# Performance work log

Measured on AMD Instinct MI355X. Metric: run time of the kernel, lower is better.

Reference implementation:

```python
import jax, jax.numpy as jnp
import numpy as np

ALPHA = 0.1        # ista() default lambda (module-level alpha is unused in this path)
N_ITERS = 50       # fixed iteration count replacing tolerance-based early exit
POWER_ITERS = 20   # power iterations to estimate Lipschitz constant L = ||Wd||_2^2


def _soft_threshold(x, t):
    return jnp.sign(x) * jnp.maximum(jnp.abs(x) - t, 0.0)


def _lipschitz(Wd):
    # largest eigenvalue of Wd^T Wd via power iteration
    v = jnp.ones((Wd.shape[1],), Wd.dtype)
    def body(v, _):
        v = Wd.T @ (Wd @ v)
        v = v / (jnp.linalg.norm(v) + 1e-12)
        return v, None
    v, _ = jax.lax.scan(body, v, None, length=POWER_ITERS)
    return jnp.vdot(v, Wd.T @ (Wd @ v)) / (jnp.vdot(v, v) + 1e-12)


def _ista(X, Wd):
    # X: [B, D], Wd: [D, K] -> sparse codes Z: [B, K]
    L = jax.lax.stop_gradient(_lipschitz(Wd))
    step = 1.0 / L
    Z0 = jnp.zeros((X.shape[0], Wd.shape[1]), X.dtype)
    def body(Z, _):
        grad = (Z @ Wd.T - X) @ Wd          # [B,D] @ [D,K] -> [B,K]
        Z = _soft_threshold(Z - step * grad, step * ALPHA)
        return Z, None
    Z, _ = jax.lax.scan(body, Z0, None, length=N_ITERS)
    return Z


def setup_inputs() -> dict:
    key = jax.random.key(0)
    k1, k2 = jax.random.split(key)
    z_e_x = jax.random.normal(k1, (8192, 16, 8, 8), jnp.float32)   # [B,C,H,W]
    dictionary = jax.random.normal(k2, (1024, 512), jnp.float32)   # [D,K], D=H*W*C
    return {"z_e_x": z_e_x, "dictionary": dictionary}


def reference(z_e_x, dictionary):
    B = z_e_x.shape[0]
    # permute(0,2,3,1).flatten(start_dim=1): [B,C,H,W] -> [B, H*W*C]
    X = jnp.transpose(z_e_x, (0, 2, 3, 1)).reshape(B, -1)
    Z = _ista(X, dictionary)                                  # [B,K]
    sparsity = jnp.sum(jnp.abs(Z) > 1e-6) / B
    outputs = (dictionary @ Z.T).T                            # [B,D]
    # torch code views back to z_e_x.shape WITHOUT inverse permute; replicate exactly
    return outputs.reshape(z_e_x.shape), sparsity
```

## Files before the change

### kernel.cpp

```cpp
#include <hip/hip_runtime.h>
#include <math.h>

#define BATCH 8192
#define DIM 1024
#define KDIM 512
#define ALPHA_C 0.1f
#define N_ITERS 50
#define ROWS 32
#define ZSH 512
#define SEG 256
#define SH 32.0f
#define SZ 16.0f
#define INVS 0.001953125f

typedef short bf16x8 __attribute__((ext_vector_type(8)));
typedef float f32x4 __attribute__((ext_vector_type(4)));
typedef long longx2 __attribute__((ext_vector_type(2)));

__device__ __forceinline__ short f2bf(float x) {
  union { float f; unsigned u; } v; v.f = x;
  unsigned r = v.u + 0x7fffu + ((v.u >> 16) & 1u);
  return (short)(r >> 16);
}
__device__ __forceinline__ float bf2f(short s) {
  union { float f; unsigned u; } v;
  v.u = ((unsigned)(unsigned short)s) << 16;
  return v.f;
}

__device__ __forceinline__ int zswz(int row, int col) {
  return row * ZSH + ((((col >> 3) ^ (row & 15)) << 3) | (col & 7));
}
__device__ __forceinline__ int zoff8(int row, int colg) {
  return row * ZSH + ((colg ^ (row & 15)) << 3);
}
__device__ __forceinline__ int z8a(int row, int c) {
  int g = ((((c >> 3) & 3) << 4) | (c >> 5)) ^ (row & 14);
  return row * 512 + g * 8 + (c & 7);
}

__global__ __launch_bounds__(256) void k_mmT_part(const float* __restrict__ A,
                                                  const float* __restrict__ B,
                                                  float* __restrict__ P) {
  int tx = (threadIdx.x & 15) * 2;
  int ty = (threadIdx.x >> 4) * 2;
  int a0 = blockIdx.y * 32 + ty;
  int b0 = blockIdx.x * 32 + tx;
  int j0 = blockIdx.z * SEG;
  float a00 = 0.f, a01 = 0.f, a10 = 0.f, a11 = 0.f;
  for (int j = j0; j < j0 + SEG; j += 8) {
#pragma unroll
    for (int u = 0; u < 8; ++u) {
      float2 av = *(const float2*)&A[(size_t)(j + u) * KDIM + a0];
      float2 bv = *(const float2*)&B[(size_t)(j + u) * KDIM + b0];
      a00 += av.x * bv.x;
      a01 += av.x * bv.y;
      a10 += av.y * bv.x;
      a11 += av.y * bv.y;
    }
  }
  float* P0 = P + (size_t)blockIdx.z * KDIM * KDIM;
  *(float2*)&P0[(size_t)a0 * KDIM + b0] = make_float2(a00, a01);
  *(float2*)&P0[(size_t)(a0 + 1) * KDIM + b0] = make_float2(a10, a11);
}

__global__ __launch_bounds__(256) void k_red(const float* __restrict__ P,
                                             float* __restrict__ C, int S,
                                             float scale) {
  int t = blockIdx.x * 256 + threadIdx.x;
  f32x4 s = (f32x4){0.f, 0.f, 0.f, 0.f};
  for (int z = 0; z < S; ++z) {
    f32x4 p = *(const f32x4*)&P[(size_t)z * KDIM * KDIM + t * 4];
    s.x += p.x; s.y += p.y; s.z += p.z; s.w += p.w;
  }
  s.x *= scale; s.y *= scale; s.z *= scale; s.w *= scale;
  *(f32x4*)&C[t * 4] = s;
}

__global__ __launch_bounds__(1024) void k_power_fast(
    const float* __restrict__ G4, const float* __restrict__ G8,
    const float* __restrict__ G, float* __restrict__ scal) {
  __shared__ float v[KDIM];
  __shared__ float part[1024];
  __shared__ double red[16];
  __shared__ double red2[16];
  __shared__ float stot;
  int tid = threadIdx.x;
  int lane = tid & 63, wid = tid >> 6;
  int col = tid & 511, h = tid >> 9;
  if (h == 0) v[col] = 1.0f;
  __syncthreads();

  const float* mats[3] = {G4, G8, G8};
#pragma unroll
  for (int s = 0; s < 3; ++s) {
    const float* gp = mats[s] + (size_t)(h * 256) * KDIM + col;
    const float* vp = v + h * 256;
    float a0 = 0.f, a1 = 0.f, a2 = 0.f, a3 = 0.f;
#pragma unroll 4
    for (int j = 0; j < 256; j += 4) {
      a0 += gp[(size_t)(j + 0) * KDIM] * vp[j + 0];
      a1 += gp[(size_t)(j + 1) * KDIM] * vp[j + 1];
      a2 += gp[(size_t)(j + 2) * KDIM] * vp[j + 2];
      a3 += gp[(size_t)(j + 3) * KDIM] * vp[j + 3];
    }
    part[tid] = (a0 + a1) + (a2 + a3);
    __syncthreads();
    float u = 0.f;
    double ssq = 0.0;
    if (h == 0) {
      u = part[col] + part[col + 512];
      ssq = (double)u * (double)u;
    }
#pragma unroll
    for (int off = 32; off; off >>= 1) ssq += __shfl_xor(ssq, off);
    if (lane == 0) red[wid] = ssq;
    __syncthreads();
    if (tid == 0) {
      double t = 0.0;
      for (int i = 0; i < 16; ++i) t += red[i];
      stot = (float)(sqrt(t) + 1e-12);
    }
    __syncthreads();
    if (h == 0) v[col] = u / stot;
    __syncthreads();
  }

  {
    const float* gp = G + (size_t)(h * 256) * KDIM + col;
    const float* vp = v + h * 256;
    float a0 = 0.f, a1 = 0.f, a2 = 0.f, a3 = 0.f;
#pragma unroll 4
    for (int j = 0; j < 256; j += 4) {
      a0 += gp[(size_t)(j + 0) * KDIM] * vp[j + 0];
      a1 += gp[(size_t)(j + 1) * KDIM] * vp[j + 1];
      a2 += gp[(size_t)(j + 2) * KDIM] * vp[j + 2];
      a3 += gp[(size_t)(j + 3) * KDIM] * vp[j + 3];
    }
    part[tid] = (a0 + a1) + (a2 + a3);
    __syncthreads();
    double nu = 0.0, de = 0.0;
    if (h == 0) {
      float u = part[col] + part[col + 512];
      nu = (double)v[col] * (double)u;
      de = (double)v[col] * (double)v[col];
    }
#pragma unroll
    for (int off = 32; off; off >>= 1) {
      nu += __shfl_xor(nu, off);
      de += __shfl_xor(de, off);
    }
    if (lane == 0) { red[wid] = nu; red2[wid] = de; }
    __syncthreads();
    if (tid == 0) {
      double n = 0.0, d = 0.0;
      for (int i = 0; i < 16; ++i) { n += red[i]; d += red2[i]; }
      float L = (float)(n / (d + 1e-12));
      float step = 1.0f / L;
      scal[0] = step;
      scal[1] = step * ALPHA_C;
    }
  }
}

__global__ __launch_bounds__(256) void k_pack_h8(const float* __restrict__ G,
                                                 const float* __restrict__ scal,
                                                 char* __restrict__ H8,
                                                 float* __restrict__ hd) {
  int t = blockIdx.x * 256 + threadIdx.x;
  int k = t >> 9, n = t & 511;
  float step = scal[0];
  float g = G[k * KDIM + n];
  if (k == n) hd[n] = 1.0f - step * g;
  float h = (k == n) ? 0.f : (-step * g) * SH;
  int p = __builtin_amdgcn_cvt_pk_fp8_f32(h, h, 0, false);
  size_t off = ((size_t)((k >> 5) * 4 + ((k >> 3) & 3))) * 4096 + n * 8 + (k & 7);
  H8[off] = (char)(p & 0xff);
}

__global__ __launch_bounds__(256) void k_pack_w(const float* __restrict__ Wd,
                                                const float* __restrict__ scal,
                                                short* __restrict__ Wh) {
  int t = blockIdx.x * 256 + threadIdx.x;
  int k = t >> 9, n = t & 511;
  float w = scal[0] * Wd[k * KDIM + n];
  int kk = k >> 5, q = (k >> 3) & 3, j = k & 7;
  Wh[((size_t)((kk * 4 + q) * 512 + n)) * 8 + j] = f2bf(w);
}

__global__ __launch_bounds__(256) void k_pack_wt(const float* __restrict__ Wd,
                                                 short* __restrict__ Wh) {
  int t = blockIdx.x * 256 + threadIdx.x;
  int k = t >> 10, n = t & 1023;
  float w = Wd[n * KDIM + k];
  int kk = k >> 5, q = (k >> 3) & 3, j = k & 7;
  Wh[((size_t)((kk * 4 + q) * 1024 + n)) * 8 + j] = f2bf(w);
}

__global__ __launch_bounds__(1024) void k_ista(
    const float* __restrict__ zex, const char* __restrict__ H8,
    const float* __restrict__ hd, const short* __restrict__ Wph,
    const short* __restrict__ Wth, const float* __restrict__ scal,
    float* __restrict__ out, int* __restrict__ gcnt) {
  __shared__ short Xb[ROWS * ZSH];
  __shared__ char Z8[2][ROWS * 512];
  int tid = threadIdx.x;
  int lane = tid & 63, wid = tid >> 6;
  int l15 = lane & 15, lq = lane >> 4;
  int rb = blockIdx.x * ROWS;
  float thr = scal[1];

  f32x4 cs[2][2];
#pragma unroll
  for (int rf = 0; rf < 2; ++rf)
#pragma unroll
    for (int cf = 0; cf < 2; ++cf) cs[rf][cf] = (f32x4){0.f, 0.f, 0.f, 0.f};

  int sr = tid >> 5;
  int sc = (tid & 31) >> 1;
  int ph = tid & 1;
  for (int half = 0; half < 2; ++half) {
    __syncthreads();
    {
      const float* src =
          &zex[(size_t)(rb + sr) * DIM + sc * 64 + half * 32 + ph * 16];
#pragma unroll
      for (int m = 0; m < 16; m += 4) {
        float4 xv = *(const float4*)&src[m];
        float xs[4] = {xv.x, xv.y, xv.z, xv.w};
#pragma unroll
        for (int e = 0; e < 4; ++e) {
          int mm = ph * 16 + m + e;
          int dd = ((mm >> 3) << 7) + ((mm & 7) << 4) + sc;
          Xb[zswz(sr, dd)] = f2bf(xs[e]);
        }
      }
    }
    __syncthreads();
#pragma unroll 2
    for (int kk = 0; kk < 16; ++kk) {
      int kkg = half * 16 + kk;
      bf16x8 a[2];
#pragma unroll
      for (int rf = 0; rf < 2; ++rf)
        a[rf] = *(const bf16x8*)&Xb[zoff8(rf * 16 + l15, kk * 4 + lq)];
#pragma unroll
      for (int cf = 0; cf < 2; ++cf) {
        int n = wid * 32 + cf * 16 + l15;
        bf16x8 bh = *(const bf16x8*)&Wph[((size_t)((kkg * 4 + lq) * 512 + n)) * 8];
#pragma unroll
        for (int rf = 0; rf < 2; ++rf)
          cs[rf][cf] = __builtin_amdgcn_mfma_f32_16x16x32_bf16(a[rf], bh, cs[rf][cf], 0, 0, 0);
      }
    }
  }
  __syncthreads();

  float hd0 = hd[wid * 32 + l15];
  float hd1 = hd[wid * 32 + 16 + l15];

  float zreg[2][2][4];
#pragma unroll
  for (int rf = 0; rf < 2; ++rf)
#pragma unroll
    for (int cf = 0; cf < 2; ++cf) {
      int col = wid * 32 + cf * 16 + l15;
#pragma unroll
      for (int e = 0; e < 4; ++e) {
        float pre = cs[rf][cf][e];
        float mag = fmaxf(fabsf(pre) - thr, 0.f);
        float z = (pre >= 0.f) ? mag : -mag;
        zreg[rf][cf][e] = z;
        int pk = __builtin_amdgcn_cvt_pk_fp8_f32(z * SZ, z * SZ, 0, false);
        Z8[0][z8a(rf * 16 + lq * 4 + e, col)] = (char)(pk & 0xff);
      }
    }
  __syncthreads();

  int key = l15 & 14;
  int abase0 = l15 * 512 + lq * 128;
  int abase1 = (16 + l15) * 512 + lq * 128;
  int vb = lq * 4096 + (wid * 32 + l15) * 8;

  int cur = 0;
#pragma unroll 1
  for (int it = 1; it < N_ITERS; ++it) {
    f32x4 acc[2][2];
#pragma unroll
    for (int rf = 0; rf < 2; ++rf)
#pragma unroll
      for (int cf = 0; cf < 2; ++cf) acc[rf][cf] = (f32x4){0.f, 0.f, 0.f, 0.f};

    int ks = (it & 7) << 1;
#define ISTA_BODY(kk)                                                         \
  {                                                                           \
    int ao = ((kk) ^ key) * 8;                                                \
    longx2 a0 = *(const longx2*)&Z8[cur][abase0 + ao];                        \
    longx2 a1 = *(const longx2*)&Z8[cur][abase1 + ao];                        \
    const char* hp = H8 + (size_t)(kk)*16384;                                 \
    long b00 = *(const long*)&hp[vb];                                         \
    long b01 = *(const long*)&hp[vb + 128];                                   \
    long b10 = *(const long*)&hp[vb + 16384];                                 \
    long b11 = *(const long*)&hp[vb + 16384 + 128];                           \
    acc[0][0] = __builtin_amdgcn_mfma_f32_16x16x32_fp8_fp8(a0.x, b00, acc[0][0], 0, 0, 0); \
    acc[1][0] = __builtin_amdgcn_mfma_f32_16x16x32_fp8_fp8(a1.x, b00, acc[1][0], 0, 0, 0); \
    acc[0][1] = __builtin_amdgcn_mfma_f32_16x16x32_fp8_fp8(a0.x, b01, acc[0][1], 0, 0, 0); \
    acc[1][1] = __builtin_amdgcn_mfma_f32_16x16x32_fp8_fp8(a1.x, b01, acc[1][1], 0, 0, 0); \
    acc[0][0] = __builtin_amdgcn_mfma_f32_16x16x32_fp8_fp8(a0.y, b10, acc[0][0], 0, 0, 0); \
    acc[1][0] = __builtin_amdgcn_mfma_f32_16x16x32_fp8_fp8(a1.y, b10, acc[1][0], 0, 0, 0); \
    acc[0][1] = __builtin_amdgcn_mfma_f32_16x16x32_fp8_fp8(a0.y, b11, acc[0][1], 0, 0, 0); \
    acc[1][1] = __builtin_amdgcn_mfma_f32_16x16x32_fp8_fp8(a1.y, b11, acc[1][1], 0, 0, 0); \
  }
#pragma unroll 1
    for (int kk = ks; kk < 16; kk += 2) ISTA_BODY(kk);
#pragma unroll 1
    for (int kk = 0; kk < ks; kk += 2) ISTA_BODY(kk);
#undef ISTA_BODY

#pragma unroll
    for (int rf = 0; rf < 2; ++rf)
#pragma unroll
      for (int cf = 0; cf < 2; ++cf) {
        float hdc = cf ? hd1 : hd0;
        int col = wid * 32 + cf * 16 + l15;
#pragma unroll
        for (int e = 0; e < 4; ++e) {
          float pre = cs[rf][cf][e] + acc[rf][cf][e] * INVS +
                      hdc * zreg[rf][cf][e];
          float mag = fmaxf(fabsf(pre) - thr, 0.f);
          float z = (pre >= 0.f) ? mag : -mag;
          zreg[rf][cf][e] = z;
          int pk = __builtin_amdgcn_cvt_pk_fp8_f32(z * SZ, z * SZ, 0, false);
          Z8[cur ^ 1][z8a(rf * 16 + lq * 4 + e, col)] = (char)(pk & 0xff);
        }
      }
    cur ^= 1;
    __syncthreads();
  }

  int cnt = 0;
#pragma unroll
  for (int rf = 0; rf < 2; ++rf)
#pragma unroll
    for (int cf = 0; cf < 2; ++cf)
#pragma unroll
      for (int e = 0; e < 4; ++e)
        cnt += (fabsf(zreg[rf][cf][e]) > 1e-6f) ? 1 : 0;
#pragma unroll
  for (int off = 32; off; off >>= 1) cnt += __shfl_xor(cnt, off);
  if (lane == 0) atomicAdd(gcnt, cnt);

#pragma unroll
  for (int rf = 0; rf < 2; ++rf)
#pragma unroll
    for (int cf = 0; cf < 2; ++cf) {
      int col = wid * 32 + cf * 16 + l15;
#pragma unroll
      for (int e = 0; e < 4; ++e)
        Xb[zswz(rf * 16 + lq * 4 + e, col)] = f2bf(zreg[rf][cf][e]);
    }
  __syncthreads();

  {
    f32x4 o[2][4];
#pragma unroll
    for (int rf = 0; rf < 2; ++rf)
#pragma unroll
      for (int cf = 0; cf < 4; ++cf) o[rf][cf] = (f32x4){0.f, 0.f, 0.f, 0.f};

#pragma unroll 2
    for (int kk = 0; kk < 16; ++kk) {
      bf16x8 a[2];
#pragma unroll
      for (int rf = 0; rf < 2; ++rf)
        a[rf] = *(const bf16x8*)&Xb[zoff8(rf * 16 + l15, kk * 4 + lq)];
#pragma unroll
      for (int cf = 0; cf < 4; ++cf) {
        int n = wid * 64 + cf * 16 + l15;
        bf16x8 bh = *(const bf16x8*)&Wth[((size_t)((kk * 4 + lq) * 1024 + n)) * 8];
#pragma unroll
        for (int rf = 0; rf < 2; ++rf)
          o[rf][cf] = __builtin_amdgcn_mfma_f32_16x16x32_bf16(a[rf], bh, o[rf][cf], 0, 0, 0);
      }
    }
#pragma unroll
    for (int rf = 0; rf < 2; ++rf)
#pragma unroll
      for (int cf = 0; cf < 4; ++cf) {
        int col = wid * 64 + cf * 16 + l15;
#pragma unroll
        for (int e = 0; e < 4; ++e) {
          int row = rb + rf * 16 + lq * 4 + e;
          out[(size_t)row * DIM + col] = o[rf][cf][e];
        }
      }
  }
}

__global__ void k_final(const int* __restrict__ gcnt, float* __restrict__ out) {
  out[(size_t)BATCH * DIM] = (float)(*gcnt) / (float)BATCH;
}

extern "C" void kernel_launch(void* const* d_in, const int* in_sizes, int n_in,
                              void* d_out, int out_size, void* d_ws,
                              size_t ws_size, hipStream_t stream) {
  (void)in_sizes; (void)n_in; (void)out_size; (void)ws_size;
  const float* zex = (const float*)d_in[0];
  const float* Wd = (const float*)d_in[1];
  float* out = (float*)d_out;
  char* ws = (char*)d_ws;

  float* G = (float*)ws;
  float* G2 = (float*)(ws + (1 << 20));
  float* G4 = (float*)(ws + 2 * (1 << 20));
  float* G8 = (float*)(ws + 3 * (1 << 20));
  char* H8 = (char*)(ws + 4 * (1 << 20));
  float* hd = (float*)(ws + 4 * (1 << 20) + (256 << 10));
  short* Wph = (short*)(ws + 4 * (1 << 20) + (512 << 10));
  short* Wth = (short*)(ws + 5 * (1 << 20) + (512 << 10));
  float* scal = (float*)(ws + 6 * (1 << 20) + (512 << 10));
  int* gcnt = (int*)(ws + 6 * (1 << 20) + (512 << 10) + 64);
  float* PG = (float*)(ws + 1 * (1 << 20));
  float* PG2 = (float*)(ws + 2 * (1 << 20));
  float* PG4 = (float*)(ws + 3 * (1 << 20));
  float* PG8 = (float*)(ws + 4 * (1 << 20));

  hipMemsetAsync(gcnt, 0, sizeof(int), stream);
  k_mmT_part<<<dim3(16, 16, 4), 256, 0, stream>>>(Wd, Wd, PG);
  k_red<<<256, 256, 0, stream>>>(PG, G, 4, 1.0f);
  k_mmT_part<<<dim3(16, 16, 2), 256, 0, stream>>>(G, G, PG2);
  k_red<<<256, 256, 0, stream>>>(PG2, G2, 2, 9.5367431640625e-07f);
  k_mmT_part<<<dim3(16, 16, 2), 256, 0, stream>>>(G2, G2, PG4);
  k_red<<<256, 256, 0, stream>>>(PG4, G4, 2, 1.0f);
  k_mmT_part<<<dim3(16, 16, 2), 256, 0, stream>>>(G4, G4, PG8);
  k_red<<<256, 256, 0, stream>>>(PG8, G8, 2, 1.0f);
  k_power_fast<<<1, 1024, 0, stream>>>(G4, G8, G, scal);
  k_pack_h8<<<1024, 256, 0, stream>>>(G, scal, H8, hd);
  k_pack_w<<<2048, 256, 0, stream>>>(Wd, scal, Wph);
  k_pack_wt<<<2048, 256, 0, stream>>>(Wd, Wth);
  k_ista<<<BATCH / ROWS, 1024, 0, stream>>>(zex, H8, hd, Wph, Wth, scal, out,
                                            gcnt);
  k_final<<<1, 1, 0, stream>>>(gcnt, out);
}
```

Measured before the change: 536.3 us.

## Compute Gram-matrix powers with bf16 MFMA and trim the setup kernel chain

Replaces the scalar fp32 split-K matmuls and reduction kernels that build G, G^2, G^4 and G^8 with a bf16 MFMA kernel that writes packed bf16 directly. G^8 is dropped, and the power iteration now applies G^4 five times. The two weight-packing kernels are merged into one that no longer depends on the step size; the step scaling moves into the ISTA kernel's epilogue. The memset is folded into the H8 pack kernel. This shortens the serial preprocessing chain and cuts launch count, at the cost of bf16 precision in the Lipschitz estimate.

```diff
diff --git a/kernel.cpp b/kernel.cpp
--- a/kernel.cpp
+++ b/kernel.cpp
@@ -8,7 +8,6 @@
 #define N_ITERS 50
 #define ROWS 32
 #define ZSH 512
-#define SEG 256
 #define SH 32.0f
 #define SZ 16.0f
 #define INVS 0.001953125f
@@ -39,47 +38,60 @@
   return row * 512 + g * 8 + (c & 7);
 }
 
-__global__ __launch_bounds__(256) void k_mmT_part(const float* __restrict__ A,
-                                                  const float* __restrict__ B,
-                                                  float* __restrict__ P) {
-  int tx = (threadIdx.x & 15) * 2;
-  int ty = (threadIdx.x >> 4) * 2;
-  int a0 = blockIdx.y * 32 + ty;
-  int b0 = blockIdx.x * 32 + tx;
-  int j0 = blockIdx.z * SEG;
-  float a00 = 0.f, a01 = 0.f, a10 = 0.f, a11 = 0.f;
-  for (int j = j0; j < j0 + SEG; j += 8) {
-#pragma unroll
-    for (int u = 0; u < 8; ++u) {
-      float2 av = *(const float2*)&A[(size_t)(j + u) * KDIM + a0];
-      float2 bv = *(const float2*)&B[(size_t)(j + u) * KDIM + b0];
-      a00 += av.x * bv.x;
-      a01 += av.x * bv.y;
-      a10 += av.y * bv.x;
-      a11 += av.y * bv.y;
-    }
-  }
-  float* P0 = P + (size_t)blockIdx.z * KDIM * KDIM;
-  *(float2*)&P0[(size_t)a0 * KDIM + b0] = make_float2(a00, a01);
-  *(float2*)&P0[(size_t)(a0 + 1) * KDIM + b0] = make_float2(a10, a11);
-}
-
-__global__ __launch_bounds__(256) void k_red(const float* __restrict__ P,
-                                             float* __restrict__ C, int S,
-                                             float scale) {
+__global__ __launch_bounds__(256) void k_pack_wd(const float* __restrict__ Wd,
+                                                 short* __restrict__ Wbh,
+                                                 short* __restrict__ Wth) {
   int t = blockIdx.x * 256 + threadIdx.x;
-  f32x4 s = (f32x4){0.f, 0.f, 0.f, 0.f};
-  for (int z = 0; z < S; ++z) {
-    f32x4 p = *(const f32x4*)&P[(size_t)z * KDIM * KDIM + t * 4];
-    s.x += p.x; s.y += p.y; s.z += p.z; s.w += p.w;
-  }
-  s.x *= scale; s.y *= scale; s.z *= scale; s.w *= scale;
-  *(f32x4*)&C[t * 4] = s;
+  if (t < DIM * KDIM) {
+    int k = t >> 9, n = t & 511;
+    int kk = k >> 5, q = (k >> 3) & 3, j = k & 7;
+    Wbh[((size_t)((kk * 4 + q) * 512 + n)) * 8 + j] = f2bf(Wd[(size_t)k * KDIM + n]);
+  } else {
+    int t2 = t - DIM * KDIM;
+    int k = t2 >> 10, n = t2 & 1023;
+    int kk = k >> 5, q = (k >> 3) & 3, j = k & 7;
+    Wth[((size_t)((kk * 4 + q) * 1024 + n)) * 8 + j] = f2bf(Wd[(size_t)n * KDIM + k]);
+  }
+}
+
+__global__ __launch_bounds__(512) void k_gemm_sym(const short* __restrict__ Af,
+                                                  int K, float scale,
+                                                  float* __restrict__ Cf32,
+                                                  short* __restrict__ Cbf) {
+  int lane = threadIdx.x & 63, wid = threadIdx.x >> 6;
+  int l15 = lane & 15, lq = lane >> 4;
+  int rt = blockIdx.x;
+  f32x4 acc[4];
+#pragma unroll
+  for (int cf = 0; cf < 4; ++cf) acc[cf] = (f32x4){0.f, 0.f, 0.f, 0.f};
+  int nk = K >> 5;
+  for (int kk = 0; kk < nk; ++kk) {
+    bf16x8 a = *(const bf16x8*)&Af[((size_t)((kk * 4 + lq) * 512 + rt * 16 + l15)) * 8];
+#pragma unroll
+    for (int cf = 0; cf < 4; ++cf) {
+      bf16x8 b = *(const bf16x8*)&Af[((size_t)((kk * 4 + lq) * 512 + wid * 64 + cf * 16 + l15)) * 8];
+      acc[cf] = __builtin_amdgcn_mfma_f32_16x16x32_bf16(a, b, acc[cf], 0, 0, 0);
+    }
+  }
+#pragma unroll
+  for (int cf = 0; cf < 4; ++cf) {
+    int col = wid * 64 + cf * 16 + l15;
+#pragma unroll
+    for (int e = 0; e < 4; ++e) {
+      int row = rt * 16 + lq * 4 + e;
+      float v = acc[cf][e] * scale;
+      if (Cf32) Cf32[(size_t)row * KDIM + col] = v;
+      if (Cbf) {
+        int kk = row >> 5, q = (row >> 3) & 3, j = row & 7;
+        Cbf[((size_t)((kk * 4 + q) * 512 + col)) * 8 + j] = f2bf(v);
+      }
+    }
+  }
 }
 
 __global__ __launch_bounds__(1024) void k_power_fast(
-    const float* __restrict__ G4, const float* __restrict__ G8,
-    const float* __restrict__ G, float* __restrict__ scal) {
+    const float* __restrict__ G4, const float* __restrict__ G,
+    float* __restrict__ scal) {
   __shared__ float v[KDIM];
   __shared__ float part[1024];
   __shared__ double red[16];
@@ -91,10 +103,8 @@
   if (h == 0) v[col] = 1.0f;
   __syncthreads();
 
-  const float* mats[3] = {G4, G8, G8};
-#pragma unroll
-  for (int s = 0; s < 3; ++s) {
-    const float* gp = mats[s] + (size_t)(h * 256) * KDIM + col;
+  for (int s = 0; s < 5; ++s) {
+    const float* gp = G4 + (size_t)(h * 256) * KDIM + col;
     const float* vp = v + h * 256;
     float a0 = 0.f, a1 = 0.f, a2 = 0.f, a3 = 0.f;
 #pragma unroll 4
@@ -166,11 +176,13 @@
 __global__ __launch_bounds__(256) void k_pack_h8(const float* __restrict__ G,
                                                  const float* __restrict__ scal,
                                                  char* __restrict__ H8,
-                                                 float* __restrict__ hd) {
+                                                 float* __restrict__ hd,
+                                                 int* __restrict__ gcnt) {
   int t = blockIdx.x * 256 + threadIdx.x;
+  if (t == 0) *gcnt = 0;
   int k = t >> 9, n = t & 511;
   float step = scal[0];
-  float g = G[k * KDIM + n];
+  float g = G[(size_t)k * KDIM + n];
   if (k == n) hd[n] = 1.0f - step * g;
   float h = (k == n) ? 0.f : (-step * g) * SH;
   int p = __builtin_amdgcn_cvt_pk_fp8_f32(h, h, 0, false);
@@ -178,28 +190,9 @@
   H8[off] = (char)(p & 0xff);
 }
 
-__global__ __launch_bounds__(256) void k_pack_w(const float* __restrict__ Wd,
-                                                const float* __restrict__ scal,
-                                                short* __restrict__ Wh) {
-  int t = blockIdx.x * 256 + threadIdx.x;
-  int k = t >> 9, n = t & 511;
-  float w = scal[0] * Wd[k * KDIM + n];
-  int kk = k >> 5, q = (k >> 3) & 3, j = k & 7;
-  Wh[((size_t)((kk * 4 + q) * 512 + n)) * 8 + j] = f2bf(w);
-}
-
-__global__ __launch_bounds__(256) void k_pack_wt(const float* __restrict__ Wd,
-                                                 short* __restrict__ Wh) {
-  int t = blockIdx.x * 256 + threadIdx.x;
-  int k = t >> 10, n = t & 1023;
-  float w = Wd[n * KDIM + k];
-  int kk = k >> 5, q = (k >> 3) & 3, j = k & 7;
-  Wh[((size_t)((kk * 4 + q) * 1024 + n)) * 8 + j] = f2bf(w);
-}
-
 __global__ __launch_bounds__(1024) void k_ista(
     const float* __restrict__ zex, const char* __restrict__ H8,
-    const float* __restrict__ hd, const short* __restrict__ Wph,
+    const float* __restrict__ hd, const short* __restrict__ Wbh,
     const short* __restrict__ Wth, const float* __restrict__ scal,
     float* __restrict__ out, int* __restrict__ gcnt) {
   __shared__ short Xb[ROWS * ZSH];
@@ -247,7 +240,7 @@
 #pragma unroll
       for (int cf = 0; cf < 2; ++cf) {
         int n = wid * 32 + cf * 16 + l15;
-        bf16x8 bh = *(const bf16x8*)&Wph[((size_t)((kkg * 4 + lq) * 512 + n)) * 8];
+        bf16x8 bh = *(const bf16x8*)&Wbh[((size_t)((kkg * 4 + lq) * 512 + n)) * 8];
 #pragma unroll
         for (int rf = 0; rf < 2; ++rf)
           cs[rf][cf] = __builtin_amdgcn_mfma_f32_16x16x32_bf16(a[rf], bh, cs[rf][cf], 0, 0, 0);
@@ -255,6 +248,12 @@
     }
   }
   __syncthreads();
+
+  float step = scal[0];
+#pragma unroll
+  for (int rf = 0; rf < 2; ++rf)
+#pragma unroll
+    for (int cf = 0; cf < 2; ++cf) cs[rf][cf] *= step;
 
   float hd0 = hd[wid * 32 + l15];
   float hd1 = hd[wid * 32 + 16 + l15];
@@ -411,34 +410,23 @@
   char* ws = (char*)d_ws;
 
   float* G = (float*)ws;
-  float* G2 = (float*)(ws + (1 << 20));
+  short* Gb = (short*)(ws + (1 << 20));
+  short* G2b = (short*)(ws + (1 << 20) + (512 << 10));
   float* G4 = (float*)(ws + 2 * (1 << 20));
-  float* G8 = (float*)(ws + 3 * (1 << 20));
-  char* H8 = (char*)(ws + 4 * (1 << 20));
-  float* hd = (float*)(ws + 4 * (1 << 20) + (256 << 10));
-  short* Wph = (short*)(ws + 4 * (1 << 20) + (512 << 10));
-  short* Wth = (short*)(ws + 5 * (1 << 20) + (512 << 10));
-  float* scal = (float*)(ws + 6 * (1 << 20) + (512 << 10));
-  int* gcnt = (int*)(ws + 6 * (1 << 20) + (512 << 10) + 64);
-  float* PG = (float*)(ws + 1 * (1 << 20));
-  float* PG2 = (float*)(ws + 2 * (1 << 20));
-  float* PG4 = (float*)(ws + 3 * (1 << 20));
-  float* PG8 = (float*)(ws + 4 * (1 << 20));
-
-  hipMemsetAsync(gcnt, 0, sizeof(int), stream);
-  k_mmT_part<<<dim3(16, 16, 4), 256, 0, stream>>>(Wd, Wd, PG);
-  k_red<<<256, 256, 0, stream>>>(PG, G, 4, 1.0f);
-  k_mmT_part<<<dim3(16, 16, 2), 256, 0, stream>>>(G, G, PG2);
-  k_red<<<256, 256, 0, stream>>>(PG2, G2, 2, 9.5367431640625e-07f);
-  k_mmT_part<<<dim3(16, 16, 2), 256, 0, stream>>>(G2, G2, PG4);
-  k_red<<<256, 256, 0, stream>>>(PG4, G4, 2, 1.0f);
-  k_mmT_part<<<dim3(16, 16, 2), 256, 0, stream>>>(G4, G4, PG8);
-  k_red<<<256, 256, 0, stream>>>(PG8, G8, 2, 1.0f);
-  k_power_fast<<<1, 1024, 0, stream>>>(G4, G8, G, scal);
-  k_pack_h8<<<1024, 256, 0, stream>>>(G, scal, H8, hd);
-  k_pack_w<<<2048, 256, 0, stream>>>(Wd, scal, Wph);
-  k_pack_wt<<<2048, 256, 0, stream>>>(Wd, Wth);
-  k_ista<<<BATCH / ROWS, 1024, 0, stream>>>(zex, H8, hd, Wph, Wth, scal, out,
+  char* H8 = (char*)(ws + 3 * (1 << 20));
+  float* hd = (float*)(ws + 3 * (1 << 20) + (256 << 10));
+  short* Wbh = (short*)(ws + 3 * (1 << 20) + (512 << 10));
+  short* Wth = (short*)(ws + 4 * (1 << 20) + (512 << 10));
+  float* scal = (float*)(ws + 5 * (1 << 20) + (512 << 10));
+  int* gcnt = (int*)(ws + 5 * (1 << 20) + (512 << 10) + 64);
+
+  k_pack_wd<<<4096, 256, 0, stream>>>(Wd, Wbh, Wth);
+  k_gemm_sym<<<32, 512, 0, stream>>>(Wbh, 1024, 1.0f, G, Gb);
+  k_gemm_sym<<<32, 512, 0, stream>>>(Gb, 512, 9.5367431640625e-07f, nullptr, G2b);
+  k_gemm_sym<<<32, 512, 0, stream>>>(G2b, 512, 1.0f, G4, nullptr);
+  k_power_fast<<<1, 1024, 0, stream>>>(G4, G, scal);
+  k_pack_h8<<<1024, 256, 0, stream>>>(G, scal, H8, hd, gcnt);
+  k_ista<<<BATCH / ROWS, 1024, 0, stream>>>(zex, H8, hd, Wbh, Wth, scal, out,
                                             gcnt);
   k_final<<<1, 1, 0, stream>>>(gcnt, out);
 }
```

Result: faster. 457.5 us (-14.7%).
